# Kernel optimization log

Measured on AMD Instinct MI355X. Metric: run time of the kernel, lower is better.

## Reference

```python
import jax, jax.numpy as jnp
import numpy as np

B, N, K, C_IN, D = 4, 2048, 16, 480, 64
EPS = 1e-5


def _c1(x, w, b):
    # 1x1 Conv1d: x (B,C,N), w (O,C) -> (B,O,N)
    return jnp.einsum('oc,bcn->bon', w, x) + b[:, None]


def _c2(x, w, b):
    # 1x1 Conv2d: x (B,C,J,N), w (O,C) -> (B,O,J,N)
    return jnp.einsum('oc,bcjn->bojn', w, x) + b[:, None, None]


def _bn(x, g, b):
    # eval-mode BatchNorm2d with running_mean=0, running_var=1
    return x * (g / jnp.sqrt(1.0 + EPS))[:, None, None] + b[:, None, None]


def _mlp_res(x, w1, b1, w2, b2, ws, bs):
    return _c1(jax.nn.relu(_c1(x, w1, b1)), w2, b2) + _c1(x, ws, bs)


def _group(f, idx):
    # f (B,C,N), idx (B,K,N) int -> out[b,c,j,n] = f[b,c,idx[b,j,n]]  -> (B,C,K,N)
    return jax.vmap(lambda ff, ii: ff[:, ii])(f, idx)


def _knn_idx(xyz):
    # xyz (B,3,N) -> idx (B,K,N), excluding the self point (nearest neighbor)
    pts = xyz.transpose(0, 2, 1)  # (B,N,3)
    sq = jnp.sum(pts * pts, -1)
    d2 = sq[:, :, None] + sq[:, None, :] - 2.0 * jnp.einsum('bnd,bmd->bnm', pts, pts)
    _, idx = jax.lax.top_k(-d2, K + 1)  # (B,N,K+1), nearest first
    return idx.transpose(0, 2, 1)[:, 1:, :]  # drop self -> (B,K,N)


def _forward(idx, feature, xyz, bt1_w, bt1_b, bt2_w, bt2_b, bts_w, bts_b,
             q_w, q_b, k_w, k_b, v_w, v_b,
             fd1_w, fd1_b, fd_g, fd_bb, fd2_w, fd2_b,
             fg1_w, fg1_b, fg_g, fg_bb, fg2_w, fg2_b,
             at_w, at_b, m41_w, m41_b, m42_w, m42_b):
    x = _mlp_res(feature, bt1_w, bt1_b, bt2_w, bt2_b, bts_w, bts_b)  # (B,64,N)
    q = _c1(x, q_w, q_b)
    k = _c1(x, k_w, k_b)
    v = _c1(x, v_w, v_b)

    group_xyz = _group(xyz, idx)                       # (B,3,K,N)
    rel_xyz = xyz[:, :, None, :] - group_xyz           # (B,3,K,N)
    pos_enc = _c2(jax.nn.relu(_bn(_c2(rel_xyz, fd1_w, fd1_b), fd_g, fd_bb)), fd2_w, fd2_b)  # (B,64,K,N)

    k_local = _group(k, idx)                           # (B,64,K,N)
    v_local = _group(v, idx)
    qk_rel = q[:, :, None, :] - k_local
    attn = _c2(jax.nn.relu(_bn(_c2(qk_rel + pos_enc, fg1_w, fg1_b), fg_g, fg_bb)), fg2_w, fg2_b)  # (B,64,K,N)

    attn1 = attn.transpose(0, 1, 3, 2)                 # (B,64,N,K)
    # ConvTranspose2d(64,64,(4,1),(4,1)) with kernel==stride: out[b,o,4n+r,f] = sum_c x[b,c,n,f]*W[c,o,r] + bias[o]
    y = jnp.einsum('bcnf,cor->bonrf', attn1, at_w)
    y = y.reshape(y.shape[0], y.shape[1], -1, y.shape[4]) + at_b[None, :, None, None]  # (B,64,4N,K)
    attn = jax.nn.softmax(y, axis=1)

    value_rel = (v_local + pos_enc).transpose(0, 1, 3, 2)   # (B,64,N,K)
    value = jnp.repeat(value_rel, 4, axis=2)                # nearest upsample (4,1) -> (B,64,4N,K)

    res = jnp.einsum('bmnf,bmnf->bmn', attn, value)         # (B,64,4N)
    identity = jnp.repeat(x, 4, axis=2)                     # nearest upsample x4 -> (B,64,4N)
    res = res + identity
    completion = _c1(jax.nn.relu(_c1(res, m41_w, m41_b)), m42_w, m42_b)  # (B,3,4N)
    return completion, res


def setup_inputs() -> dict:
    key = jax.random.key(0)
    ks = jax.random.split(key, 24)
    i = iter(range(24))

    def w(shape):
        return (jax.random.normal(ks[next(i)], shape, dtype=jnp.float32) * 0.05)

    z = lambda n: jnp.zeros((n,), jnp.float32)
    o = lambda n: jnp.ones((n,), jnp.float32)
    return {
        'feature': jax.random.normal(ks[next(i)], (B, C_IN, N), dtype=jnp.float32),
        'xyz': jax.random.normal(ks[next(i)], (B, 3, N), dtype=jnp.float32),
        'bt1_w': w((D, C_IN)), 'bt1_b': z(D),
        'bt2_w': w((D, D)), 'bt2_b': z(D),
        'bts_w': w((D, C_IN)), 'bts_b': z(D),
        'q_w': w((D, D)), 'q_b': z(D),
        'k_w': w((D, D)), 'k_b': z(D),
        'v_w': w((D, D)), 'v_b': z(D),
        'fd1_w': w((D, 3)), 'fd1_b': z(D), 'fd_g': o(D), 'fd_bb': z(D),
        'fd2_w': w((D, D)), 'fd2_b': z(D),
        'fg1_w': w((4 * D, D)), 'fg1_b': z(4 * D), 'fg_g': o(4 * D), 'fg_bb': z(4 * D),
        'fg2_w': w((D, 4 * D)), 'fg2_b': z(D),
        'at_w': w((D, D, 4)), 'at_b': z(D),
        'm41_w': w((D, D)), 'm41_b': z(D),
        'm42_w': w((3, D)), 'm42_b': z(3),
    }


def reference(feature, xyz, bt1_w, bt1_b, bt2_w, bt2_b, bts_w, bts_b,
              q_w, q_b, k_w, k_b, v_w, v_b,
              fd1_w, fd1_b, fd_g, fd_bb, fd2_w, fd2_b,
              fg1_w, fg1_b, fg_g, fg_bb, fg2_w, fg2_b,
              at_w, at_b, m41_w, m41_b, m42_w, m42_b):
    idx = _knn_idx(xyz)
    return _forward(idx, feature, xyz, bt1_w, bt1_b, bt2_w, bt2_b, bts_w, bts_b,
                    q_w, q_b, k_w, k_b, v_w, v_b,
                    fd1_w, fd1_b, fd_g, fd_bb, fd2_w, fd2_b,
                    fg1_w, fg1_b, fg_g, fg_bb, fg2_w, fg2_b,
                    at_w, at_b, m41_w, m41_b, m42_w, m42_b)
```

## Files before the change

kernel.cpp:

```cpp
#include <hip/hip_runtime.h>

#define B_ 4
#define N_ 2048
#define K_ 16
#define CIN_ 480
#define UPN_ 8192
#define M_ (B_*N_*K_)
#define MX_ (B_*N_)
#define KCAP 448

typedef unsigned int u32;
typedef unsigned short u16;
typedef unsigned long long u64;
typedef __attribute__((ext_vector_type(8))) short short8;
typedef __attribute__((ext_vector_type(4))) float f32x4;

#define DEV static __device__ __forceinline__

DEV float b2f(u16 h){ return __uint_as_float(((u32)h)<<16); }
DEV u16 f2b(float f){
  u32 u = __float_as_uint(f);
  u32 r = u + 0x7fffu + ((u>>16)&1u);
  return (u16)(r>>16);
}
DEV u32 cvtpk(float a, float b){
  u32 r; asm("v_cvt_pk_bf16_f32 %0, %1, %2" : "=v"(r) : "v"(a), "v"(b));
  return r;
}
DEV u64 cvtpk4(float a, float b, float c, float d){
  return (u64)cvtpk(a,b) | ((u64)cvtpk(c,d)<<32);
}
DEV bool detect_bf(const void* fg){ return ((((const u32*)fg)[0]) & 0xFFFFu) == 0x3F80u; }
DEV float ld(const void* p, int i, bool bf){
  return bf ? b2f(((const u16*)p)[i]) : ((const float*)p)[i];
}
DEV u64 makekey(float d2, int m){
  u32 bits = __float_as_uint(d2);
  bits = (bits & 0x80000000u) ? ~bits : (bits | 0x80000000u);
  return ((u64)bits<<32) | (u32)m;
}
DEV int swz64 (int row, int colByte){ return row*128 + (colByte ^ ((row&7)<<4)); }
DEV int swz128(int row, int colByte){ return row*256 + (colByte ^ ((row&7)<<4)); }

__global__ __launch_bounds__(256) void transpose_kernel(const void* __restrict__ feature,
    const void* __restrict__ fg, u16* __restrict__ fxbT)
{
  __shared__ u16 s[32][34];
  bool bf = detect_bf(fg);
  int ntile = blockIdx.x, ctile = blockIdx.y, b = blockIdx.z;
  int tx = threadIdx.x & 31, ty = threadIdx.x >> 5;
  u64 base = (u64)b*CIN_*N_;
  #pragma unroll
  for(int r=0;r<4;r++){
    int c = ctile*32 + ty + r*8;
    int n = ntile*32 + tx;
    u64 i = base + (u64)c*N_ + n;
    s[ty + r*8][tx] = bf ? ((const u16*)feature)[i] : f2b(((const float*)feature)[i]);
  }
  __syncthreads();
  #pragma unroll
  for(int r=0;r<4;r++){
    int nl = ty + r*8;
    int n = ntile*32 + nl;
    fxbT[(u64)b*N_*CIN_ + (u64)n*CIN_ + ctile*32 + tx] = s[tx][nl];
  }
}

__global__ __launch_bounds__(256) void prep_kernel(
    const void* __restrict__ bt1_w, const void* __restrict__ bt1_b,
    const void* __restrict__ bt2_w, const void* __restrict__ bt2_b,
    const void* __restrict__ bts_w, const void* __restrict__ bts_b,
    const void* __restrict__ q_w, const void* __restrict__ q_b,
    const void* __restrict__ k_w, const void* __restrict__ k_b,
    const void* __restrict__ v_w, const void* __restrict__ v_b,
    const void* __restrict__ fd1_w, const void* __restrict__ fd1_b,
    const void* __restrict__ fd_g, const void* __restrict__ fd_bb,
    const void* __restrict__ fd2_w, const void* __restrict__ fd2_b,
    const void* __restrict__ fg1_w, const void* __restrict__ fg1_b,
    const void* __restrict__ fg_g, const void* __restrict__ fg_bb,
    const void* __restrict__ fg2_w, const void* __restrict__ fg2_b,
    const void* __restrict__ at_w, const void* __restrict__ at_b,
    const void* __restrict__ m41_w, const void* __restrict__ m41_b,
    const void* __restrict__ m42_w, const void* __restrict__ m42_b,
    float* __restrict__ W, u16* __restrict__ WB)
{
  int t = blockIdx.x*256 + threadIdx.x;
  bool bf = detect_bf(fd_g);
  const float inv = 0.9999950000374997f;
  if(t < 30720) return; t -= 30720;
  if(t < 30720) return; t -= 30720;
  if(t < 4096) return; t -= 4096;
  if(t < 4096) return; t -= 4096;
  if(t < 4096) return; t -= 4096;
  if(t < 4096) return; t -= 4096;
  if(t < 256){
    int o=t>>2, j=t&3; float s = ld(fd_g,o,bf)*inv;
    W[77824+t] = (j<3) ? s*ld(fd1_w,o*3+j,bf) : (s*ld(fd1_b,o,bf) + ld(fd_bb,o,bf));
    return;
  } t -= 256;
  if(t < 4096) return; t -= 4096;
  if(t < 16384) return; t -= 16384;
  if(t < 256){ float s=ld(fg_g,t,bf)*inv; W[98560+t] = s*ld(fg1_b,t,bf) + ld(fg_bb,t,bf); return; } t -= 256;
  if(t < 16384) return; t -= 16384;
  if(t < 16384) return; t -= 16384;
  if(t < 4096){ int m=t>>6, o=t&63; W[131584+t] = ld(m41_w,o*64+m,bf); return; } t -= 4096;
  if(t < 192){ W[135680+t] = ld(m42_w,t,bf); return; } t -= 192;
  if(t < 64){ W[135872+t] = ld(bt1_b,t,bf); return; } t -= 64;
  if(t < 64){ W[135936+t] = ld(bts_b,t,bf); return; } t -= 64;
  if(t < 64){ W[136000+t] = ld(bt2_b,t,bf); return; } t -= 64;
  if(t < 64){ W[136064+t] = ld(q_b,t,bf); return; } t -= 64;
  if(t < 64){ W[136128+t] = ld(k_b,t,bf); return; } t -= 64;
  if(t < 64){ W[136192+t] = ld(v_b,t,bf); return; } t -= 64;
  if(t < 64){ W[136256+t] = ld(fd2_b,t,bf); return; } t -= 64;
  if(t < 64){ W[136320+t] = ld(fg2_b,t,bf); return; } t -= 64;
  if(t < 64){ W[136384+t] = ld(at_b,t,bf); return; } t -= 64;
  if(t < 64){ W[136448+t] = ld(m41_b,t,bf); return; } t -= 64;
  if(t < 3){ W[136512+t] = ld(m42_b,t,bf); return; } t -= 3;
  if(t < 16384){ int o=t>>6; float s=ld(fg_g,o,bf)*inv; WB[t] = f2b(s*ld(fg1_w,t,bf)); return; } t -= 16384;
  if(t < 16384){ WB[16384+t] = f2b(ld(fg2_w,t,bf)); return; } t -= 16384;
  if(t < 16384){ int j=t>>6, c=t&63;
                 WB[32768+t] = f2b(ld(at_w,(c*64+(j&63))*4+(j>>6),bf)); return; } t -= 16384;
  if(t < 256){ W[136576+t] = ld(at_b,t&63,bf); return; } t -= 256;
  if(t < 4096){ WB[49152+t] = f2b(ld(fd2_w,t,bf)); return; } t -= 4096;
  if(t < 30720){ WB[53248+t] = f2b(ld(bt1_w,t,bf)); return; } t -= 30720;
  if(t < 30720){ WB[83968+t] = f2b(ld(bts_w,t,bf)); return; } t -= 30720;
  if(t < 4096){ WB[114688+t] = f2b(ld(bt2_w,t,bf)); return; } t -= 4096;
  if(t < 4096){ WB[118784+t] = f2b(ld(q_w,t,bf)); return; } t -= 4096;
  if(t < 4096){ WB[122880+t] = f2b(ld(k_w,t,bf)); return; } t -= 4096;
  if(t < 4096){ WB[126976+t] = f2b(ld(v_w,t,bf)); return; }
}

__global__ __launch_bounds__(256) void knn_kernel(const void* __restrict__ xyz,
    const void* __restrict__ fg, float* __restrict__ fxyz, int* __restrict__ idx)
{
  __shared__ float px[N_], py[N_], pz[N_], sq[N_];
  __shared__ u64 sbuf[4][KCAP];
  __shared__ u64 smin[4][64];
  __shared__ int scnt[4][64];
  __shared__ u64 stau[4];
  int b = blockIdx.y;
  bool bf = detect_bf(fg);
  int base = b*3*N_;
  bool w0 = (blockIdx.x==0);
  for(int i=threadIdx.x;i<N_;i+=256){
    float xx=ld(xyz,base+i,bf), yy=ld(xyz,base+N_+i,bf), zz=ld(xyz,base+2*N_+i,bf);
    px[i]=xx; py[i]=yy; pz[i]=zz; sq[i]=xx*xx+yy*yy+zz*zz;
    if(w0){ fxyz[base+i]=xx; fxyz[base+N_+i]=yy; fxyz[base+2*N_+i]=zz; }
  }
  __syncthreads();
  int w = threadIdx.x>>6, l = threadIdx.x&63;
  int q = blockIdx.x*4 + w;
  float qx=px[q], qy=py[q], qz=pz[q], qs=sq[q];
  float d2c[32];
  u64 best=~0ull;
  #pragma unroll
  for(int j=0;j<32;j++){
    int m = l*32 + ((j+l)&31);
    float d2 = (qs+sq[m]) - 2.0f*(qx*px[m]+qy*py[m]+qz*pz[m]);
    d2c[j]=d2;
    u64 key = makekey(d2, m);
    best = key<best ? key : best;
  }
  smin[w][l]=best;
  __syncthreads();
  {
    int rank=0;
    for(int i=0;i<64;i++) rank += (smin[w][i] < best);
    if(rank==16) stau[w] = best;
  }
  __syncthreads();
  u64 tau = stau[w];
  int myc=0;
  #pragma unroll
  for(int j=0;j<32;j++){
    int m = l*32 + ((j+l)&31);
    myc += (makekey(d2c[j], m) <= tau);
  }
  scnt[w][l]=myc;
  __syncthreads();
  int off=0, tot=0;
  for(int i=0;i<64;i++){
    int c = scnt[w][i];
    tot += c;
    off += (i<l) ? c : 0;
  }
  #pragma unroll
  for(int j=0;j<32;j++){
    int m = l*32 + ((j+l)&31);
    u64 key = makekey(d2c[j], m);
    if(key<=tau && off<KCAP){ sbuf[w][off]=key; off++; }
  }
  __syncthreads();
  if(tot>KCAP) tot=KCAP;
  for(int p=l; p<tot; p+=64){
    u64 kk = sbuf[w][p];
    int rk=0;
    for(int i=0;i<tot;i++) rk += (sbuf[w][i] < kk);
    if(rk>=1 && rk<17) idx[(b*K_+(rk-1))*N_+q] = ((int)(kk & 0xffffffffu)) & (N_-1);
  }
}

__global__ __launch_bounds__(256) void gemm480_mfma(const u16* __restrict__ A,
    const u16* __restrict__ Wt, const float* __restrict__ bias,
    u16* __restrict__ hout, float* __restrict__ xsout)
{
  int tid=threadIdx.x, w=tid>>6, lane=tid&63;
  int rbase=(blockIdx.x*4+w)*16;
  int cbase=blockIdx.y*64;
  int lr=lane&15, lk=(lane>>4)*8;
  f32x4 acc[4];
  #pragma unroll
  for(int j=0;j<4;j++) acc[j]=(f32x4){0.f,0.f,0.f,0.f};
  for(int kc=0;kc<CIN_;kc+=32){
    short8 a = *(const short8*)(A + (u64)(rbase+lr)*CIN_ + kc + lk);
    #pragma unroll
    for(int tj=0;tj<4;tj++){
      short8 bb = *(const short8*)(Wt + (u64)(cbase+tj*16+lr)*CIN_ + kc + lk);
      acc[tj] = __builtin_amdgcn_mfma_f32_16x16x32_bf16(a, bb, acc[tj], 0,0,0);
    }
  }
  int rq=(lane>>4)*4;
  #pragma unroll
  for(int tj=0;tj<4;tj++){
    int col = cbase + tj*16 + lr;
    float bv = bias[col];
    #pragma unroll
    for(int reg=0;reg<4;reg++){
      u64 row = rbase + rq + reg;
      float vv = acc[tj][reg] + bv;
      if(blockIdx.y==0) hout[row*64 + col] = f2b(fmaxf(vv,0.f));
      else              xsout[row*64 + (col-64)] = vv;
    }
  }
}

__global__ __launch_bounds__(256) void x_mfma(const u16* __restrict__ A,
    const u16* __restrict__ Wt, const float* __restrict__ bias,
    const float* __restrict__ xs, float* __restrict__ x, u16* __restrict__ xb)
{
  int tid=threadIdx.x, w=tid>>6, lane=tid&63;
  int rbase=(blockIdx.x*4+w)*16;
  int lr=lane&15, lk=(lane>>4)*8;
  f32x4 acc[4];
  #pragma unroll
  for(int j=0;j<4;j++) acc[j]=(f32x4){0.f,0.f,0.f,0.f};
  #pragma unroll
  for(int kc=0;kc<64;kc+=32){
    short8 a = *(const short8*)(A + (u64)(rbase+lr)*64 + kc + lk);
    #pragma unroll
    for(int tj=0;tj<4;tj++){
      short8 bb = *(const short8*)(Wt + (u64)(tj*16+lr)*64 + kc + lk);
      acc[tj] = __builtin_amdgcn_mfma_f32_16x16x32_bf16(a, bb, acc[tj], 0,0,0);
    }
  }
  int rq=(lane>>4)*4;
  #pragma unroll
  for(int tj=0;tj<4;tj++){
    int col = tj*16 + lr;
    float bv = bias[col];
    #pragma unroll
    for(int reg=0;reg<4;reg++){
      u64 row = rbase + rq + reg;
      float vv = acc[tj][reg] + bv + xs[row*64+col];
      x[row*64+col] = vv;
      xb[row*64+col] = f2b(vv);
    }
  }
}

__global__ __launch_bounds__(256) void qkv_mfma(const u16* __restrict__ A,
    const u16* __restrict__ Wt, const float* __restrict__ bias, float* __restrict__ qkv)
{
  int tid=threadIdx.x, w=tid>>6, lane=tid&63;
  int rbase=(blockIdx.x*4+w)*16;
  int cbase=blockIdx.y*64;
  int lr=lane&15, lk=(lane>>4)*8;
  f32x4 acc[4];
  #pragma unroll
  for(int j=0;j<4;j++) acc[j]=(f32x4){0.f,0.f,0.f,0.f};
  #pragma unroll
  for(int kc=0;kc<64;kc+=32){
    short8 a = *(const short8*)(A + (u64)(rbase+lr)*64 + kc + lk);
    #pragma unroll
    for(int tj=0;tj<4;tj++){
      short8 bb = *(const short8*)(Wt + (u64)(cbase+tj*16+lr)*64 + kc + lk);
      acc[tj] = __builtin_amdgcn_mfma_f32_16x16x32_bf16(a, bb, acc[tj], 0,0,0);
    }
  }
  int rq=(lane>>4)*4;
  #pragma unroll
  for(int tj=0;tj<4;tj++){
    int col = cbase + tj*16 + lr;
    float bv = bias[col];
    #pragma unroll
    for(int reg=0;reg<4;reg++){
      u64 row = rbase + rq + reg;
      qkv[row*192 + col] = acc[tj][reg] + bv;
    }
  }
}

__global__ __launch_bounds__(256) void fused_chain(
    const int* __restrict__ idx, const float* __restrict__ fxyz,
    const float* __restrict__ qkv, const float* __restrict__ x,
    const float* __restrict__ fd1f,
    const u16* __restrict__ Wfd2, const float* __restrict__ bfd2,
    const u16* __restrict__ Wfg1, const float* __restrict__ bfg1,
    const u16* __restrict__ Wfg2, const float* __restrict__ bfg2,
    const u16* __restrict__ Wat,  const float* __restrict__ bat,
    const void* __restrict__ det, void* __restrict__ out)
{
  __shared__ alignas(16) unsigned char lds[32768];
  int tid = threadIdx.x;
  int w = tid>>6, lane = tid&63;
  int lr = lane&15, lk = (lane>>4)*8, rq = (lane>>4)*4;

  int erow = tid>>2, ecg = tid&3;
  int el = erow>>4, ef = erow&15;
  int bn_e = blockIdx.x*4 + el;
  int b_e = bn_e>>11, n_e = bn_e&(N_-1);
  int jn = idx[(b_e*K_+ef)*N_ + n_e] & (N_-1);

  {
    const float* xb = fxyz + (u64)b_e*3*N_;
    float rx = xb[n_e]      - xb[jn];
    float ry = xb[N_+n_e]   - xb[N_+jn];
    float rz = xb[2*N_+n_e] - xb[2*N_+jn];
    #pragma unroll
    for(int gg=0; gg<4; gg++){
      float tv[4];
      #pragma unroll
      for(int j=0;j<4;j++){
        f32x4 wv = *(const f32x4*)(fd1f + ((ecg*4+gg)*4+j)*4);
        tv[j] = fmaxf(wv[0]*rx + wv[1]*ry + wv[2]*rz + wv[3], 0.f);
      }
      *(u64*)(lds + swz64(erow, (ecg*4+gg)*8)) = cvtpk4(tv[0],tv[1],tv[2],tv[3]);
    }
  }
  __syncthreads();

  {
    f32x4 acc[4];
    #pragma unroll
    for(int i=0;i<4;i++) acc[i]=(f32x4){0.f,0.f,0.f,0.f};
    #pragma unroll
    for(int kc=0;kc<64;kc+=32){
      short8 wf = *(const short8*)(Wfd2 + (u64)(w*16+lr)*64 + kc + lk);
      #pragma unroll
      for(int ti=0;ti<4;ti++){
        short8 tf = *(const short8*)(lds + swz64(ti*16+lr, (kc+lk)*2));
        acc[ti] = __builtin_amdgcn_mfma_f32_16x16x32_bf16(wf, tf, acc[ti], 0,0,0);
      }
    }
    f32x4 b4 = *(const f32x4*)(bfd2 + w*16 + rq);
    #pragma unroll
    for(int ti=0;ti<4;ti++)
      *(u64*)(lds + 8192 + swz64(ti*16+lr, (w*16+rq)*2)) =
        cvtpk4(acc[ti][0]+b4[0], acc[ti][1]+b4[1], acc[ti][2]+b4[2], acc[ti][3]+b4[3]);
  }
  __syncthreads();

  {
    int mg = ecg*16;
    const float* qrow = qkv + (u64)(b_e*N_+n_e)*192 + mg;
    const float* krow = qkv + (u64)(b_e*N_+jn)*192 + 64 + mg;
    const float* vrow = qkv + (u64)(b_e*N_+jn)*192 + 128 + mg;
    #pragma unroll
    for(int g2=0; g2<4; g2++){
      f32x4 qv = *(const f32x4*)(qrow + g2*4);
      f32x4 kv = *(const f32x4*)(krow + g2*4);
      f32x4 vv = *(const f32x4*)(vrow + g2*4);
      int cb = (mg + g2*4)*2;
      u64 pw = *(const u64*)(lds + 8192 + swz64(erow, cb));
      float p0=b2f((u16)pw), p1=b2f((u16)(pw>>16)), p2=b2f((u16)(pw>>32)), p3=b2f((u16)(pw>>48));
      *(u64*)(lds + swz64(erow, cb)) =
        cvtpk4(qv[0]-kv[0]+p0, qv[1]-kv[1]+p1, qv[2]-kv[2]+p2, qv[3]-kv[3]+p3);
      *(u64*)(lds + 8192 + swz64(erow, cb)) =
        cvtpk4(vv[0]+p0, vv[1]+p1, vv[2]+p2, vv[3]+p3);
    }
  }
  __syncthreads();

  float vreg[16];
  #pragma unroll
  for(int f2=0; f2<16; f2++)
    vreg[f2] = b2f(*(const u16*)(lds + 8192 + swz64(w*16+f2, lane*2)));

  f32x4 gacc[4];
  #pragma unroll
  for(int i=0;i<4;i++) gacc[i]=(f32x4){0.f,0.f,0.f,0.f};
  #pragma unroll
  for(int half=0; half<2; half++){
    {
      f32x4 hacc[2][4];
      #pragma unroll
      for(int i=0;i<2;i++)
        #pragma unroll
        for(int j=0;j<4;j++) hacc[i][j]=(f32x4){0.f,0.f,0.f,0.f};
      #pragma unroll
      for(int kc=0;kc<64;kc+=32){
        short8 wf[2], af[4];
        #pragma unroll
        for(int ti=0;ti<2;ti++)
          wf[ti] = *(const short8*)(Wfg1 + (u64)(half*128 + w*32 + ti*16 + lr)*64 + kc + lk);
        #pragma unroll
        for(int tj=0;tj<4;tj++)
          af[tj] = *(const short8*)(lds + swz64(tj*16+lr, (kc+lk)*2));
        #pragma unroll
        for(int ti=0;ti<2;ti++)
          #pragma unroll
          for(int tj=0;tj<4;tj++)
            hacc[ti][tj] = __builtin_amdgcn_mfma_f32_16x16x32_bf16(wf[ti], af[tj], hacc[ti][tj], 0,0,0);
      }
      #pragma unroll
      for(int ti=0;ti<2;ti++){
        f32x4 b4 = *(const f32x4*)(bfg1 + half*128 + w*32 + ti*16 + rq);
        #pragma unroll
        for(int tj=0;tj<4;tj++){
          int row = tj*16 + lr;
          *(u64*)(lds + 16384 + swz128(row, (w*32+ti*16+rq)*2)) =
            cvtpk4(fmaxf(hacc[ti][tj][0]+b4[0],0.f), fmaxf(hacc[ti][tj][1]+b4[1],0.f),
                   fmaxf(hacc[ti][tj][2]+b4[2],0.f), fmaxf(hacc[ti][tj][3]+b4[3],0.f));
        }
      }
    }
    __syncthreads();
    #pragma unroll
    for(int kc=0;kc<128;kc+=32){
      short8 wf = *(const short8*)(Wfg2 + (u64)(w*16+lr)*256 + half*128 + kc + lk);
      #pragma unroll
      for(int tj=0;tj<4;tj++){
        short8 hf = *(const short8*)(lds + 16384 + swz128(tj*16+lr, (kc+lk)*2));
        gacc[tj] = __builtin_amdgcn_mfma_f32_16x16x32_bf16(wf, hf, gacc[tj], 0,0,0);
      }
    }
    __syncthreads();
  }

  {
    f32x4 b4 = *(const f32x4*)(bfg2 + w*16 + rq);
    #pragma unroll
    for(int tj=0;tj<4;tj++)
      *(u64*)(lds + swz64(tj*16+lr, (w*16+rq)*2)) =
        cvtpk4(gacc[tj][0]+b4[0], gacc[tj][1]+b4[1], gacc[tj][2]+b4[2], gacc[tj][3]+b4[3]);
  }
  __syncthreads();

  float aout[4];
  int srow = tid>>2, sub = tid&3;
  #pragma unroll
  for(int r=0;r<4;r++){
    {
      f32x4 acc[4];
      #pragma unroll
      for(int i=0;i<4;i++) acc[i]=(f32x4){0.f,0.f,0.f,0.f};
      #pragma unroll
      for(int kc=0;kc<64;kc+=32){
        short8 wf = *(const short8*)(Wat + (u64)(r*64 + w*16 + lr)*64 + kc + lk);
        #pragma unroll
        for(int tj=0;tj<4;tj++){
          short8 gf = *(const short8*)(lds + swz64(tj*16+lr, (kc+lk)*2));
          acc[tj] = __builtin_amdgcn_mfma_f32_16x16x32_bf16(wf, gf, acc[tj], 0,0,0);
        }
      }
      f32x4 b4 = *(const f32x4*)(bat + r*64 + w*16 + rq);
      #pragma unroll
      for(int tj=0;tj<4;tj++)
        *(u64*)(lds + 16384 + swz64(tj*16+lr, (w*16+rq)*2)) =
          cvtpk4(acc[tj][0]+b4[0], acc[tj][1]+b4[1], acc[tj][2]+b4[2], acc[tj][3]+b4[3]);
    }
    __syncthreads();
    {
      float yv[16];
      uint4 pk0 = *(const uint4*)(lds + 16384 + swz64(srow, sub*32));
      uint4 pk1 = *(const uint4*)(lds + 16384 + swz64(srow, sub*32 + 16));
      yv[0]=__uint_as_float(pk0.x<<16); yv[1]=__uint_as_float(pk0.x&0xffff0000u);
      yv[2]=__uint_as_float(pk0.y<<16); yv[3]=__uint_as_float(pk0.y&0xffff0000u);
      yv[4]=__uint_as_float(pk0.z<<16); yv[5]=__uint_as_float(pk0.z&0xffff0000u);
      yv[6]=__uint_as_float(pk0.w<<16); yv[7]=__uint_as_float(pk0.w&0xffff0000u);
      yv[8]=__uint_as_float(pk1.x<<16); yv[9]=__uint_as_float(pk1.x&0xffff0000u);
      yv[10]=__uint_as_float(pk1.y<<16); yv[11]=__uint_as_float(pk1.y&0xffff0000u);
      yv[12]=__uint_as_float(pk1.z<<16); yv[13]=__uint_as_float(pk1.z&0xffff0000u);
      yv[14]=__uint_as_float(pk1.w<<16); yv[15]=__uint_as_float(pk1.w&0xffff0000u);
      float mx = yv[0];
      #pragma unroll
      for(int m=1;m<16;m++) mx = fmaxf(mx, yv[m]);
      mx = fmaxf(mx, __shfl_xor(mx, 1));
      mx = fmaxf(mx, __shfl_xor(mx, 2));
      float sm = 0.f;
      #pragma unroll
      for(int m=0;m<16;m++){ float e = __expf(yv[m]-mx); yv[m]=e; sm+=e; }
      sm += __shfl_xor(sm, 1);
      sm += __shfl_xor(sm, 2);
      float rinv = 1.0f/sm;
      uint4 o0, o1;
      o0.x = cvtpk(yv[0]*rinv, yv[1]*rinv);  o0.y = cvtpk(yv[2]*rinv, yv[3]*rinv);
      o0.z = cvtpk(yv[4]*rinv, yv[5]*rinv);  o0.w = cvtpk(yv[6]*rinv, yv[7]*rinv);
      o1.x = cvtpk(yv[8]*rinv, yv[9]*rinv);  o1.y = cvtpk(yv[10]*rinv, yv[11]*rinv);
      o1.z = cvtpk(yv[12]*rinv, yv[13]*rinv); o1.w = cvtpk(yv[14]*rinv, yv[15]*rinv);
      *(uint4*)(lds + 8192 + swz64(srow, sub*32))      = o0;
      *(uint4*)(lds + 8192 + swz64(srow, sub*32 + 16)) = o1;
    }
    __syncthreads();
    {
      float a = 0.f;
      #pragma unroll
      for(int f2=0; f2<16; f2++)
        a += b2f(*(const u16*)(lds + 8192 + swz64(w*16+f2, lane*2))) * vreg[f2];
      aout[r] = a;
    }
  }

  int bn = blockIdx.x*4 + w;
  int b = bn>>11, n = bn&(N_-1);
  float xv = x[(u64)bn*64 + lane];
  u64 off = 98304 + ((u64)(b*64+lane))*UPN_ + (u64)n*4;
  if(detect_bf(det)){
    *(u64*)((u16*)out + off) = cvtpk4(aout[0]+xv, aout[1]+xv, aout[2]+xv, aout[3]+xv);
  } else {
    f32x4 pk = {aout[0]+xv, aout[1]+xv, aout[2]+xv, aout[3]+xv};
    *(f32x4*)((float*)out + off) = pk;
  }
}

__global__ __launch_bounds__(128) void comp_kernel(
  const float* __restrict__ m41T, const float* __restrict__ m41b,
  const float* __restrict__ m42f, const float* __restrict__ m42b,
  const void* __restrict__ det, void* __restrict__ out)
{
  int t = blockIdx.x*128 + threadIdx.x;
  int un = t & (UPN_-1);
  int b = t >> 13;
  bool bf = detect_bf(det);
  float acc[64];
  #pragma unroll
  for(int o=0;o<64;o++) acc[o] = m41b[o];
  if(bf){
    const u16* rr = (const u16*)out + 98304 + (u64)b*64*UPN_ + un;
    for(int c=0;c<64;c++){
      float rv = b2f(rr[(u64)c*UPN_]);
      const float* w = m41T + c*64;
      #pragma unroll
      for(int o=0;o<64;o++) acc[o] += w[o]*rv;
    }
  } else {
    const float* rr = (const float*)out + 98304 + (u64)b*64*UPN_ + un;
    for(int c=0;c<64;c++){
      float rv = rr[(u64)c*UPN_];
      const float* w = m41T + c*64;
      #pragma unroll
      for(int o=0;o<64;o++) acc[o] += w[o]*rv;
    }
  }
  float c0=m42b[0], c1=m42b[1], c2=m42b[2];
  #pragma unroll
  for(int o=0;o<64;o++){
    float hv = fmaxf(acc[o],0.f);
    c0 += m42f[o]*hv; c1 += m42f[64+o]*hv; c2 += m42f[128+o]*hv;
  }
  u64 base = (u64)b*3*UPN_ + un;
  if(bf){
    u16* cp = (u16*)out;
    cp[base]=f2b(c0); cp[base+UPN_]=f2b(c1); cp[base+2*UPN_]=f2b(c2);
  } else {
    float* cp = (float*)out;
    cp[base]=c0; cp[base+UPN_]=c1; cp[base+2*UPN_]=c2;
  }
}

extern "C" void kernel_launch(void* const* d_in, const int* in_sizes, int n_in,
                              void* d_out, int out_size, void* d_ws, size_t ws_size,
                              hipStream_t stream)
{
  (void)in_sizes; (void)n_in; (void)out_size; (void)ws_size;
  const void* feature=d_in[0];
  const void* xyz   =d_in[1];
  const void* bt1_w =d_in[2];  const void* bt1_b=d_in[3];
  const void* bt2_w =d_in[4];  const void* bt2_b=d_in[5];
  const void* bts_w =d_in[6];  const void* bts_b=d_in[7];
  const void* q_w   =d_in[8];  const void* q_b =d_in[9];
  const void* k_w   =d_in[10]; const void* k_b =d_in[11];
  const void* v_w   =d_in[12]; const void* v_b =d_in[13];
  const void* fd1_w =d_in[14]; const void* fd1_b=d_in[15];
  const void* fd_g  =d_in[16]; const void* fd_bb=d_in[17];
  const void* fd2_w =d_in[18]; const void* fd2_b=d_in[19];
  const void* fg1_w =d_in[20]; const void* fg1_b=d_in[21];
  const void* fg_g  =d_in[22]; const void* fg_bb=d_in[23];
  const void* fg2_w =d_in[24]; const void* fg2_b=d_in[25];
  const void* at_w  =d_in[26]; const void* at_b =d_in[27];
  const void* m41_w =d_in[28]; const void* m41_b=d_in[29];
  const void* m42_w =d_in[30]; const void* m42_b=d_in[31];

  char* ws=(char*)d_ws;
  float* W   =(float*)(ws);
  u16*  WB   =(u16*)  (ws + 589824);
  int*  idx  =(int*)  (ws + 851968);
  float* x   =(float*)(ws + 1376256);
  float* qkv =(float*)(ws + 3473408);
  u16*  h    =(u16*)  (ws + 9764864);
  float* xs  =(float*)(ws + 10813440);
  u16*  xb   =(u16*)  (ws + 12910592);
  u16*  fxbT =(u16*)  (ws + 114622464);
  float* fxyz=(float*)(ws + 122486784);

  const float* W_fd1f = W+77824;
  const float* W_fg1fb= W+98560;
  const float* W_m41T = W+131584;
  const float* W_m42  = W+135680;
  const float* Wb_g480= W+135872;
  const float* Wb_bt2 = W+136000;
  const float* Wb_qkv = W+136064;
  const float* Wb_fd2 = W+136256;
  const float* Wb_fg2 = W+136320;
  const float* Wb_m41 = W+136448;
  const float* Wb_m42 = W+136512;
  const float* W_atb256 = W+136576;
  const u16* WB_fg1  = WB;
  const u16* WB_fg2  = WB+16384;
  const u16* WB_at   = WB+32768;
  const u16* WB_fd2  = WB+49152;
  const u16* WB_g480 = WB+53248;
  const u16* WB_bt2  = WB+114688;
  const u16* WB_qkv  = WB+118784;

  prep_kernel<<<1047,256,0,stream>>>(bt1_w,bt1_b,bt2_w,bt2_b,bts_w,bts_b,q_w,q_b,k_w,k_b,
      v_w,v_b,fd1_w,fd1_b,fd_g,fd_bb,fd2_w,fd2_b,fg1_w,fg1_b,fg_g,fg_bb,fg2_w,fg2_b,
      at_w,at_b,m41_w,m41_b,m42_w,m42_b,W,WB);
  transpose_kernel<<<dim3(64,15,4),256,0,stream>>>(feature, fd_g, fxbT);
  knn_kernel<<<dim3(N_/4,B_),256,0,stream>>>(xyz, fd_g, fxyz, idx);
  gemm480_mfma<<<dim3(MX_/64,2),256,0,stream>>>(fxbT, WB_g480, Wb_g480, h, xs);
  x_mfma<<<MX_/64,256,0,stream>>>(h, WB_bt2, Wb_bt2, xs, x, xb);
  qkv_mfma<<<dim3(MX_/64,3),256,0,stream>>>(xb, WB_qkv, Wb_qkv, qkv);
  fused_chain<<<B_*N_/4,256,0,stream>>>(idx, fxyz, qkv, x, W_fd1f,
      WB_fd2, Wb_fd2, WB_fg1, W_fg1fb, WB_fg2, Wb_fg2, WB_at, W_atb256, fd_g, d_out);
  comp_kernel<<<256,128,0,stream>>>(W_m41T, Wb_m41, W_m42, Wb_m42, fd_g, d_out);
}
```

Measured before the change: 267.8 us.

## Merge prep, transpose and kNN into one launch; hoist LDS fragments; split comp outputs

Three independent setup kernels (weight prep, feature transpose, kNN) become one launch that dispatches on block index, removing two launches and letting the independent work share the GPU. The transpose now moves 64 points per tile with paired u32 loads and stores. In fused_chain, the LDS B-operand fragments for the fg1 and at GEMMs are loaded once into registers instead of reloading them inside loops, trading extra VGPRs for fewer LDS reads. comp_kernel splits the 64 output channels across two half-waves combined with a shuffle, doubling the thread count and halving per-thread registers. The merged kernel carries the kNN kernel's ~50KB LDS footprint for every block, which may reduce occupancy for the transpose and prep blocks.

```diff
diff --git a/kernel.cpp b/kernel.cpp
--- a/kernel.cpp
+++ b/kernel.cpp
@@ -9,6 +9,10 @@
 #define MX_ (B_*N_)
 #define KCAP 448
 
+#define KNN_BLK 2048
+#define TR_BLK  1920
+#define PREP_BLK 1047
+
 typedef unsigned int u32;
 typedef unsigned short u16;
 typedef unsigned long long u64;
@@ -42,31 +46,8 @@
 DEV int swz64 (int row, int colByte){ return row*128 + (colByte ^ ((row&7)<<4)); }
 DEV int swz128(int row, int colByte){ return row*256 + (colByte ^ ((row&7)<<4)); }
 
-__global__ __launch_bounds__(256) void transpose_kernel(const void* __restrict__ feature,
-    const void* __restrict__ fg, u16* __restrict__ fxbT)
-{
-  __shared__ u16 s[32][34];
-  bool bf = detect_bf(fg);
-  int ntile = blockIdx.x, ctile = blockIdx.y, b = blockIdx.z;
-  int tx = threadIdx.x & 31, ty = threadIdx.x >> 5;
-  u64 base = (u64)b*CIN_*N_;
-  #pragma unroll
-  for(int r=0;r<4;r++){
-    int c = ctile*32 + ty + r*8;
-    int n = ntile*32 + tx;
-    u64 i = base + (u64)c*N_ + n;
-    s[ty + r*8][tx] = bf ? ((const u16*)feature)[i] : f2b(((const float*)feature)[i]);
-  }
-  __syncthreads();
-  #pragma unroll
-  for(int r=0;r<4;r++){
-    int nl = ty + r*8;
-    int n = ntile*32 + nl;
-    fxbT[(u64)b*N_*CIN_ + (u64)n*CIN_ + ctile*32 + tx] = s[tx][nl];
-  }
-}
-
-__global__ __launch_bounds__(256) void prep_kernel(
+__global__ __launch_bounds__(256) void setup_kernel(
+    const void* __restrict__ feature, const void* __restrict__ xyz,
     const void* __restrict__ bt1_w, const void* __restrict__ bt1_b,
     const void* __restrict__ bt2_w, const void* __restrict__ bt2_b,
     const void* __restrict__ bts_w, const void* __restrict__ bts_b,
@@ -82,10 +63,118 @@
     const void* __restrict__ at_w, const void* __restrict__ at_b,
     const void* __restrict__ m41_w, const void* __restrict__ m41_b,
     const void* __restrict__ m42_w, const void* __restrict__ m42_b,
-    float* __restrict__ W, u16* __restrict__ WB)
+    float* __restrict__ W, u16* __restrict__ WB,
+    u16* __restrict__ fxbT, float* __restrict__ fxyz, int* __restrict__ idx)
 {
-  int t = blockIdx.x*256 + threadIdx.x;
+  __shared__ alignas(16) unsigned char smem[50208];
+  int blkid = blockIdx.x;
   bool bf = detect_bf(fd_g);
+
+  if(blkid < KNN_BLK){
+    float* px = (float*)smem;
+    float* py = px + N_;
+    float* pz = py + N_;
+    float* sq = pz + N_;
+    u64*  sbuf = (u64*)(sq + N_);
+    u64*  smin = sbuf + 4*KCAP;
+    int*  scnt = (int*)(smin + 256);
+    u64*  stau = (u64*)(scnt + 256);
+    int bx = blkid & 511;
+    int b = blkid >> 9;
+    int base = b*3*N_;
+    bool w0 = (bx==0);
+    for(int i=threadIdx.x;i<N_;i+=256){
+      float xx=ld(xyz,base+i,bf), yy=ld(xyz,base+N_+i,bf), zz=ld(xyz,base+2*N_+i,bf);
+      px[i]=xx; py[i]=yy; pz[i]=zz; sq[i]=xx*xx+yy*yy+zz*zz;
+      if(w0){ fxyz[base+i]=xx; fxyz[base+N_+i]=yy; fxyz[base+2*N_+i]=zz; }
+    }
+    __syncthreads();
+    int w = threadIdx.x>>6, l = threadIdx.x&63;
+    int q = bx*4 + w;
+    float qx=px[q], qy=py[q], qz=pz[q], qs=sq[q];
+    float d2c[32];
+    u64 best=~0ull;
+    #pragma unroll
+    for(int j=0;j<32;j++){
+      int m = l*32 + ((j+l)&31);
+      float d2 = (qs+sq[m]) - 2.0f*(qx*px[m]+qy*py[m]+qz*pz[m]);
+      d2c[j]=d2;
+      u64 key = makekey(d2, m);
+      best = key<best ? key : best;
+    }
+    smin[w*64+l]=best;
+    __syncthreads();
+    {
+      int rank=0;
+      for(int i=0;i<64;i++) rank += (smin[w*64+i] < best);
+      if(rank==16) stau[w] = best;
+    }
+    __syncthreads();
+    u64 tau = stau[w];
+    int myc=0;
+    #pragma unroll
+    for(int j=0;j<32;j++){
+      int m = l*32 + ((j+l)&31);
+      myc += (makekey(d2c[j], m) <= tau);
+    }
+    scnt[w*64+l]=myc;
+    __syncthreads();
+    int off=0, tot=0;
+    for(int i=0;i<64;i++){
+      int c = scnt[w*64+i];
+      tot += c;
+      off += (i<l) ? c : 0;
+    }
+    #pragma unroll
+    for(int j=0;j<32;j++){
+      int m = l*32 + ((j+l)&31);
+      u64 key = makekey(d2c[j], m);
+      if(key<=tau && off<KCAP){ sbuf[w*KCAP+off]=key; off++; }
+    }
+    __syncthreads();
+    if(tot>KCAP) tot=KCAP;
+    for(int p=l; p<tot; p+=64){
+      u64 kk = sbuf[w*KCAP+p];
+      int rk=0;
+      for(int i=0;i<tot;i++) rk += (sbuf[w*KCAP+i] < kk);
+      if(rk>=1 && rk<17) idx[(b*K_+(rk-1))*N_+q] = ((int)(kk & 0xffffffffu)) & (N_-1);
+    }
+    return;
+  }
+
+  if(blkid < KNN_BLK + TR_BLK){
+    u16 (*s)[34] = (u16(*)[34])smem;
+    int t = blkid - KNN_BLK;
+    int ntile = t & 31;  int rest = t >> 5;
+    int ctile = rest % 15; int b = rest / 15;
+    int tx = threadIdx.x & 31, ty = threadIdx.x >> 5;
+    u64 base = (u64)b*CIN_*N_;
+    #pragma unroll
+    for(int r=0;r<4;r++){
+      int c = ctile*32 + ty + r*8;
+      u64 i = base + (u64)c*N_ + ntile*64 + tx*2;
+      u32 v;
+      if(bf) v = *(const u32*)((const u16*)feature + i);
+      else {
+        float a0=((const float*)feature)[i], a1=((const float*)feature)[i+1];
+        v = (u32)f2b(a0) | ((u32)f2b(a1)<<16);
+      }
+      s[tx*2  ][ty + r*8] = (u16)v;
+      s[tx*2+1][ty + r*8] = (u16)(v>>16);
+    }
+    __syncthreads();
+    #pragma unroll
+    for(int r=0;r<4;r++){
+      int i2 = r*256 + threadIdx.x;
+      int nrow = i2 >> 4, cp = i2 & 15;
+      u32 v = *(const u32*)&s[nrow][cp*2];
+      int n = ntile*64 + nrow;
+      *(u32*)(fxbT + (u64)b*N_*CIN_ + (u64)n*CIN_ + ctile*32 + cp*2) = v;
+    }
+    return;
+  }
+
+  int t = (blkid - (KNN_BLK + TR_BLK))*256 + threadIdx.x;
   const float inv = 0.9999950000374997f;
   if(t < 30720) return; t -= 30720;
   if(t < 30720) return; t -= 30720;
@@ -130,76 +219,6 @@
   if(t < 4096){ WB[126976+t] = f2b(ld(v_w,t,bf)); return; }
 }
 
-__global__ __launch_bounds__(256) void knn_kernel(const void* __restrict__ xyz,
-    const void* __restrict__ fg, float* __restrict__ fxyz, int* __restrict__ idx)
-{
-  __shared__ float px[N_], py[N_], pz[N_], sq[N_];
-  __shared__ u64 sbuf[4][KCAP];
-  __shared__ u64 smin[4][64];
-  __shared__ int scnt[4][64];
-  __shared__ u64 stau[4];
-  int b = blockIdx.y;
-  bool bf = detect_bf(fg);
-  int base = b*3*N_;
-  bool w0 = (blockIdx.x==0);
-  for(int i=threadIdx.x;i<N_;i+=256){
-    float xx=ld(xyz,base+i,bf), yy=ld(xyz,base+N_+i,bf), zz=ld(xyz,base+2*N_+i,bf);
-    px[i]=xx; py[i]=yy; pz[i]=zz; sq[i]=xx*xx+yy*yy+zz*zz;
-    if(w0){ fxyz[base+i]=xx; fxyz[base+N_+i]=yy; fxyz[base+2*N_+i]=zz; }
-  }
-  __syncthreads();
-  int w = threadIdx.x>>6, l = threadIdx.x&63;
-  int q = blockIdx.x*4 + w;
-  float qx=px[q], qy=py[q], qz=pz[q], qs=sq[q];
-  float d2c[32];
-  u64 best=~0ull;
-  #pragma unroll
-  for(int j=0;j<32;j++){
-    int m = l*32 + ((j+l)&31);
-    float d2 = (qs+sq[m]) - 2.0f*(qx*px[m]+qy*py[m]+qz*pz[m]);
-    d2c[j]=d2;
-    u64 key = makekey(d2, m);
-    best = key<best ? key : best;
-  }
-  smin[w][l]=best;
-  __syncthreads();
-  {
-    int rank=0;
-    for(int i=0;i<64;i++) rank += (smin[w][i] < best);
-    if(rank==16) stau[w] = best;
-  }
-  __syncthreads();
-  u64 tau = stau[w];
-  int myc=0;
-  #pragma unroll
-  for(int j=0;j<32;j++){
-    int m = l*32 + ((j+l)&31);
-    myc += (makekey(d2c[j], m) <= tau);
-  }
-  scnt[w][l]=myc;
-  __syncthreads();
-  int off=0, tot=0;
-  for(int i=0;i<64;i++){
-    int c = scnt[w][i];
-    tot += c;
-    off += (i<l) ? c : 0;
-  }
-  #pragma unroll
-  for(int j=0;j<32;j++){
-    int m = l*32 + ((j+l)&31);
-    u64 key = makekey(d2c[j], m);
-    if(key<=tau && off<KCAP){ sbuf[w][off]=key; off++; }
-  }
-  __syncthreads();
-  if(tot>KCAP) tot=KCAP;
-  for(int p=l; p<tot; p+=64){
-    u64 kk = sbuf[w][p];
-    int rk=0;
-    for(int i=0;i<tot;i++) rk += (sbuf[w][i] < kk);
-    if(rk>=1 && rk<17) idx[(b*K_+(rk-1))*N_+q] = ((int)(kk & 0xffffffffu)) & (N_-1);
-  }
-}
-
 __global__ __launch_bounds__(256) void gemm480_mfma(const u16* __restrict__ A,
     const u16* __restrict__ Wt, const float* __restrict__ bias,
     u16* __restrict__ hout, float* __restrict__ xsout)
@@ -386,6 +405,13 @@
   for(int f2=0; f2<16; f2++)
     vreg[f2] = b2f(*(const u16*)(lds + 8192 + swz64(w*16+f2, lane*2)));
 
+  short8 ainf[2][4];
+  #pragma unroll
+  for(int kc2=0;kc2<2;kc2++)
+    #pragma unroll
+    for(int tj=0;tj<4;tj++)
+      ainf[kc2][tj] = *(const short8*)(lds + swz64(tj*16+lr, (kc2*32+lk)*2));
+
   f32x4 gacc[4];
   #pragma unroll
   for(int i=0;i<4;i++) gacc[i]=(f32x4){0.f,0.f,0.f,0.f};
@@ -398,19 +424,16 @@
         #pragma unroll
         for(int j=0;j<4;j++) hacc[i][j]=(f32x4){0.f,0.f,0.f,0.f};
       #pragma unroll
-      for(int kc=0;kc<64;kc+=32){
-        short8 wf[2], af[4];
+      for(int kc2=0;kc2<2;kc2++){
+        short8 wf[2];
         #pragma unroll
         for(int ti=0;ti<2;ti++)
-          wf[ti] = *(const short8*)(Wfg1 + (u64)(half*128 + w*32 + ti*16 + lr)*64 + kc + lk);
-        #pragma unroll
-        for(int tj=0;tj<4;tj++)
-          af[tj] = *(const short8*)(lds + swz64(tj*16+lr, (kc+lk)*2));
+          wf[ti] = *(const short8*)(Wfg1 + (u64)(half*128 + w*32 + ti*16 + lr)*64 + kc2*32 + lk);
         #pragma unroll
         for(int ti=0;ti<2;ti++)
           #pragma unroll
           for(int tj=0;tj<4;tj++)
-            hacc[ti][tj] = __builtin_amdgcn_mfma_f32_16x16x32_bf16(wf[ti], af[tj], hacc[ti][tj], 0,0,0);
+            hacc[ti][tj] = __builtin_amdgcn_mfma_f32_16x16x32_bf16(wf[ti], ainf[kc2][tj], hacc[ti][tj], 0,0,0);
       }
       #pragma unroll
       for(int ti=0;ti<2;ti++){
@@ -446,6 +469,13 @@
   }
   __syncthreads();
 
+  short8 gfr[2][4];
+  #pragma unroll
+  for(int kc2=0;kc2<2;kc2++)
+    #pragma unroll
+    for(int tj=0;tj<4;tj++)
+      gfr[kc2][tj] = *(const short8*)(lds + swz64(tj*16+lr, (kc2*32+lk)*2));
+
   float aout[4];
   int srow = tid>>2, sub = tid&3;
   #pragma unroll
@@ -455,13 +485,11 @@
       #pragma unroll
       for(int i=0;i<4;i++) acc[i]=(f32x4){0.f,0.f,0.f,0.f};
       #pragma unroll
-      for(int kc=0;kc<64;kc+=32){
-        short8 wf = *(const short8*)(Wat + (u64)(r*64 + w*16 + lr)*64 + kc + lk);
+      for(int kc2=0;kc2<2;kc2++){
+        short8 wf = *(const short8*)(Wat + (u64)(r*64 + w*16 + lr)*64 + kc2*32 + lk);
         #pragma unroll
-        for(int tj=0;tj<4;tj++){
-          short8 gf = *(const short8*)(lds + swz64(tj*16+lr, (kc+lk)*2));
-          acc[tj] = __builtin_amdgcn_mfma_f32_16x16x32_bf16(wf, gf, acc[tj], 0,0,0);
-        }
+        for(int tj=0;tj<4;tj++)
+          acc[tj] = __builtin_amdgcn_mfma_f32_16x16x32_bf16(wf, gfr[kc2][tj], acc[tj], 0,0,0);
       }
       f32x4 b4 = *(const f32x4*)(bat + r*64 + w*16 + rq);
       #pragma unroll
@@ -528,43 +556,52 @@
   const float* __restrict__ m42f, const float* __restrict__ m42b,
   const void* __restrict__ det, void* __restrict__ out)
 {
-  int t = blockIdx.x*128 + threadIdx.x;
-  int un = t & (UPN_-1);
-  int b = t >> 13;
+  int tid = threadIdx.x;
+  int wv = tid>>6, lane = tid&63;
+  int half = lane>>5, l32 = lane&31;
+  int g = blockIdx.x*64 + wv*32 + l32;
+  int un = g & (UPN_-1);
+  int b = g >> 13;
   bool bf = detect_bf(det);
-  float acc[64];
-  #pragma unroll
-  for(int o=0;o<64;o++) acc[o] = m41b[o];
+  float acc[32];
+  #pragma unroll
+  for(int o=0;o<32;o++) acc[o] = m41b[half*32+o];
   if(bf){
     const u16* rr = (const u16*)out + 98304 + (u64)b*64*UPN_ + un;
     for(int c=0;c<64;c++){
       float rv = b2f(rr[(u64)c*UPN_]);
-      const float* w = m41T + c*64;
-      #pragma unroll
-      for(int o=0;o<64;o++) acc[o] += w[o]*rv;
+      const float* w = m41T + c*64 + half*32;
+      #pragma unroll
+      for(int o=0;o<32;o++) acc[o] += w[o]*rv;
     }
   } else {
     const float* rr = (const float*)out + 98304 + (u64)b*64*UPN_ + un;
     for(int c=0;c<64;c++){
       float rv = rr[(u64)c*UPN_];
-      const float* w = m41T + c*64;
-      #pragma unroll
-      for(int o=0;o<64;o++) acc[o] += w[o]*rv;
-    }
-  }
-  float c0=m42b[0], c1=m42b[1], c2=m42b[2];
-  #pragma unroll
-  for(int o=0;o<64;o++){
+      const float* w = m41T + c*64 + half*32;
+      #pragma unroll
+      for(int o=0;o<32;o++) acc[o] += w[o]*rv;
+    }
+  }
+  float c0=0.f, c1=0.f, c2=0.f;
+  #pragma unroll
+  for(int o=0;o<32;o++){
     float hv = fmaxf(acc[o],0.f);
-    c0 += m42f[o]*hv; c1 += m42f[64+o]*hv; c2 += m42f[128+o]*hv;
-  }
-  u64 base = (u64)b*3*UPN_ + un;
-  if(bf){
-    u16* cp = (u16*)out;
-    cp[base]=f2b(c0); cp[base+UPN_]=f2b(c1); cp[base+2*UPN_]=f2b(c2);
-  } else {
-    float* cp = (float*)out;
-    cp[base]=c0; cp[base+UPN_]=c1; cp[base+2*UPN_]=c2;
+    c0 += m42f[half*32+o]*hv; c1 += m42f[64+half*32+o]*hv; c2 += m42f[128+half*32+o]*hv;
+  }
+  c0 += __shfl_xor(c0, 32);
+  c1 += __shfl_xor(c1, 32);
+  c2 += __shfl_xor(c2, 32);
+  if(half==0){
+    c0 += m42b[0]; c1 += m42b[1]; c2 += m42b[2];
+    u64 base = (u64)b*3*UPN_ + un;
+    if(bf){
+      u16* cp = (u16*)out;
+      cp[base]=f2b(c0); cp[base+UPN_]=f2b(c1); cp[base+2*UPN_]=f2b(c2);
+    } else {
+      float* cp = (float*)out;
+      cp[base]=c0; cp[base+UPN_]=c1; cp[base+2*UPN_]=c2;
+    }
   }
 }
 
@@ -623,15 +660,14 @@
   const u16* WB_bt2  = WB+114688;
   const u16* WB_qkv  = WB+118784;
 
-  prep_kernel<<<1047,256,0,stream>>>(bt1_w,bt1_b,bt2_w,bt2_b,bts_w,bts_b,q_w,q_b,k_w,k_b,
+  setup_kernel<<<KNN_BLK+TR_BLK+PREP_BLK,256,0,stream>>>(feature, xyz,
+      bt1_w,bt1_b,bt2_w,bt2_b,bts_w,bts_b,q_w,q_b,k_w,k_b,
       v_w,v_b,fd1_w,fd1_b,fd_g,fd_bb,fd2_w,fd2_b,fg1_w,fg1_b,fg_g,fg_bb,fg2_w,fg2_b,
-      at_w,at_b,m41_w,m41_b,m42_w,m42_b,W,WB);
-  transpose_kernel<<<dim3(64,15,4),256,0,stream>>>(feature, fd_g, fxbT);
-  knn_kernel<<<dim3(N_/4,B_),256,0,stream>>>(xyz, fd_g, fxyz, idx);
+      at_w,at_b,m41_w,m41_b,m42_w,m42_b,W,WB,fxbT,fxyz,idx);
   gemm480_mfma<<<dim3(MX_/64,2),256,0,stream>>>(fxbT, WB_g480, Wb_g480, h, xs);
   x_mfma<<<MX_/64,256,0,stream>>>(h, WB_bt2, Wb_bt2, xs, x, xb);
   qkv_mfma<<<dim3(MX_/64,3),256,0,stream>>>(xb, WB_qkv, Wb_qkv, qkv);
   fused_chain<<<B_*N_/4,256,0,stream>>>(idx, fxyz, qkv, x, W_fd1f,
       WB_fd2, Wb_fd2, WB_fg1, W_fg1fb, WB_fg2, Wb_fg2, WB_at, W_atb256, fd_g, d_out);
-  comp_kernel<<<256,128,0,stream>>>(W_m41T, Wb_m41, W_m42, Wb_m42, fd_g, d_out);
-}
+  comp_kernel<<<512,128,0,stream>>>(W_m41T, Wb_m41, W_m42, Wb_m42, fd_g, d_out);
+}
```

Result: slower. 277.5 us (+3.6%).
